# Kernel tuning notes

Measured on AMD Instinct MI355X. Metric: run time of the kernel, lower is better.

The kernel has to match this reference:

```python
import jax, jax.numpy as jnp
import numpy as np


def setup_inputs() -> dict:
    key = jax.random.key(0)
    k1, k2, k3, k4 = jax.random.split(key, 4)
    B, S, D = 32, 2048, 128
    queries = jax.random.normal(k1, (B, S, D), dtype=jnp.float32)
    keys = jax.random.normal(k2, (B, S, D), dtype=jnp.float32)
    values = jax.random.normal(k3, (B, S, D), dtype=jnp.float32)
    mask = jax.random.randint(k4, (B, 1, S), 0, 2, dtype=jnp.int32)
    return {"queries": queries, "keys": keys, "values": values, "mask": mask}


def reference(queries, keys, values, mask):
    # scores: [B, Sq, Sk]
    scores = jnp.einsum("bqd,bkd->bqk", queries, keys)
    pad = (mask == 0)  # broadcasts [B,1,Sk] over queries
    min_value = jnp.finfo(scores.dtype).min
    scores = jnp.where(pad, min_value, scores)
    attn = jax.nn.softmax(scores, axis=-1)
    attn = jnp.where(pad, jnp.array(0.0, attn.dtype), attn)
    return jnp.einsum("bqk,bkd->bqd", attn, values)
```

## Files before the change

kernel.cpp:

```cpp
#include <hip/hip_runtime.h>
#include <stdint.h>

#define Bb 32
#define Ss 2048
#define Dd 128
#define KVB 64
#define NIT (Ss / KVB)

typedef __attribute__((ext_vector_type(2))) float f32x2;
typedef __attribute__((ext_vector_type(4))) float f32x4;
typedef __attribute__((ext_vector_type(16))) float f32x16;
typedef __attribute__((ext_vector_type(8))) _Float16 f16x8;
typedef __attribute__((ext_vector_type(2))) __fp16 fp16x2;
typedef __attribute__((ext_vector_type(8))) unsigned short u16x8;
typedef __attribute__((ext_vector_type(4))) unsigned short u16x4;

union F16_8 { u16x8 u; uint32_t w[4]; f16x8 h; };
union F16_4 { u16x4 u; uint32_t w[2]; };

__device__ __forceinline__ uint32_t pk2(float a, float b) {
    union { fp16x2 h; uint32_t u; } v;
    v.h = __builtin_amdgcn_cvt_pkrtz(a, b);
    return v.u;
}

__global__ __launch_bounds__(256)
void attn_compact_idx(const int* __restrict__ M, int* __restrict__ IDXg, int* __restrict__ CNT) {
    __shared__ int scan_s[256];
    const int b = blockIdx.x, tid = threadIdx.x;
    const int* m = M + (size_t)b * Ss + tid * 8;
    int loc[8]; int csum = 0;
    {
        int4 a = *(const int4*)m;
        int4 c = *(const int4*)(m + 4);
        loc[0] = (a.x != 0); loc[1] = (a.y != 0); loc[2] = (a.z != 0); loc[3] = (a.w != 0);
        loc[4] = (c.x != 0); loc[5] = (c.y != 0); loc[6] = (c.z != 0); loc[7] = (c.w != 0);
#pragma unroll
        for (int j = 0; j < 8; ++j) csum += loc[j];
    }
    scan_s[tid] = csum;
    __syncthreads();
    for (int off = 1; off < 256; off <<= 1) {
        int v = scan_s[tid];
        int u = (tid >= off) ? scan_s[tid - off] : 0;
        __syncthreads();
        scan_s[tid] = v + u;
        __syncthreads();
    }
    int base = scan_s[tid] - csum;
    int* idx = IDXg + (size_t)b * Ss;
#pragma unroll
    for (int j = 0; j < 8; ++j)
        if (loc[j]) idx[base++] = tid * 8 + j;
    if (tid == 255) CNT[b] = scan_s[255];
}

__global__ __launch_bounds__(256)
void attn_compact_copy(const float* __restrict__ K, const float* __restrict__ V,
                       const int* __restrict__ IDXg, const int* __restrict__ CNT,
                       unsigned short* __restrict__ Kc, unsigned short* __restrict__ Vc) {
    const int b = blockIdx.x >> 5, chunk = blockIdx.x & 31;
    const int count = CNT[b];
    const int ntpad = ((count + 63) >> 6) << 6;
    const int p0 = chunk * 64;
    if (p0 >= ntpad) return;
    const int tid  = threadIdx.x;
    const int rsub = tid >> 4;
    const int colh = (tid & 15) * 8;
    const int* idx = IDXg + (size_t)b * Ss;
    const size_t gbase = (size_t)b * Ss * Dd;
#pragma unroll
    for (int pass = 0; pass < 2; ++pass) {
        const float* src = pass ? V : K;
        unsigned short* dst = pass ? Vc : Kc;
#pragma unroll
        for (int it = 0; it < 4; ++it) {
            int s = p0 + rsub + it * 16;
            if (s >= ntpad) continue;
            F16_8 t;
            if (s < count) {
                const float* sp = src + gbase + (size_t)idx[s] * Dd + colh;
                f32x4 x = *(const f32x4*)sp;
                f32x4 y = *(const f32x4*)(sp + 4);
                t.w[0] = pk2(x[0], x[1]); t.w[1] = pk2(x[2], x[3]);
                t.w[2] = pk2(y[0], y[1]); t.w[3] = pk2(y[2], y[3]);
            } else {
                t.w[0] = 0u; t.w[1] = 0u; t.w[2] = 0u; t.w[3] = 0u;
            }
            *(u16x8*)(dst + gbase + (size_t)s * Dd + colh) = t.u;
        }
    }
}

__global__ __launch_bounds__(256) __attribute__((amdgpu_waves_per_eu(2, 2)))
void attn_fwd_c(const float* __restrict__ Q,
                const unsigned short* __restrict__ Kc,
                const unsigned short* __restrict__ Vc,
                const int* __restrict__ CNT,
                float* __restrict__ O) {
    __shared__ unsigned short K_lds[KVB * 128];
    __shared__ unsigned short VT_lds[128 * 64];
    __shared__ float maskadd[KVB];

    const int tid = threadIdx.x;
    const int w   = tid >> 6;
    const int l   = tid & 63;
    const int q31 = l & 31;
    const int hi  = l >> 5;

    const int bid   = blockIdx.x;
    const int batch = (bid & 7) * 4 + (bid >> 7);
    const int qtile = (bid >> 3) & 15;

    const size_t qrow0 = (size_t)batch * Ss + qtile * 128 + w * 32;
    const size_t kvb16 = (size_t)batch * Ss * Dd;

    const int count = CNT[batch];
    const int ntile = (count + KVB - 1) >> 6;

    const int krow  = tid >> 4;
    const int kcol8 = (tid & 15) << 3;
    const int vi    = tid & 15;
    const int vk    = (tid >> 4) << 2;

    u16x8    ka[4];
    uint32_t vv[4][4];

    auto issueK = [&](int kv) {
#pragma unroll
        for (int it = 0; it < 4; ++it)
            ka[it] = *(const u16x8*)(Kc + kvb16 + (size_t)(kv + krow + it * 16) * Dd + kcol8);
    };
    auto writeK = [&](int kv) {
#pragma unroll
        for (int it = 0; it < 4; ++it) {
            int row = krow + it * 16;
            *(u16x8*)&K_lds[(row * 128 + kcol8) ^ ((row & 7) << 3)] = ka[it];
        }
        if (tid < KVB) maskadd[tid] = (kv + tid < count) ? 0.f : -1e30f;
    };
    auto issueV = [&](int kv) {
#pragma unroll
        for (int j = 0; j < 4; ++j)
#pragma unroll
            for (int ko = 0; ko < 4; ++ko)
                vv[j][ko] = *(const uint32_t*)(Vc + kvb16 + (size_t)(kv + vk + ko) * Dd + 2 * vi + 32 * j);
    };
    auto writeV = [&]() {
#pragma unroll
        for (int j = 0; j < 4; ++j)
#pragma unroll
            for (int p = 0; p < 2; ++p) {
                int row = 2 * vi + p + 32 * j;
                F16_4 t;
                if (p == 0) {
                    t.w[0] = (vv[j][0] & 0xffffu) | (vv[j][1] << 16);
                    t.w[1] = (vv[j][2] & 0xffffu) | (vv[j][3] << 16);
                } else {
                    t.w[0] = (vv[j][0] >> 16) | (vv[j][1] & 0xffff0000u);
                    t.w[1] = (vv[j][2] >> 16) | (vv[j][3] & 0xffff0000u);
                }
                *(u16x4*)&VT_lds[row * 64 + (vk ^ ((row & 7) << 3))] = t.u;
            }
    };

    F16_8 ones;
    {
        uint32_t ow = (q31 < 8) ? 0x3C003C00u : 0u;
        ones.w[0] = ow; ones.w[1] = ow; ones.w[2] = ow; ones.w[3] = ow;
    }

    const f32x16 z16 = {0,0,0,0,0,0,0,0,0,0,0,0,0,0,0,0};
    f32x16 acco[4];
#pragma unroll
    for (int dn = 0; dn < 4; ++dn) acco[dn] = z16;
    f32x16 accl = z16;
    float mrun = -1e4f;

    const float LOG2E = 1.44269504088896340736f;
    if (ntile > 0) { issueK(0); issueV(0); }
    F16_8 qf[8];
#pragma unroll
    for (int ks = 0; ks < 8; ++ks) {
        const float* s = Q + (qrow0 + q31) * Dd + ks * 16 + hi * 8;
        f32x4 a = *(const f32x4*)s;
        f32x4 b = *(const f32x4*)(s + 4);
        qf[ks].w[0] = pk2(a[0] * LOG2E, a[1] * LOG2E);
        qf[ks].w[1] = pk2(a[2] * LOG2E, a[3] * LOG2E);
        qf[ks].w[2] = pk2(b[0] * LOG2E, b[1] * LOG2E);
        qf[ks].w[3] = pk2(b[2] * LOG2E, b[3] * LOG2E);
    }
    if (ntile > 0) {
        writeK(0); writeV();
        __syncthreads();
    }

    for (int t = 0; t < ntile; ++t) {
        if (t < ntile - 1) issueK((t + 1) * KVB);

        f32x16 accs[2];
        accs[0] = z16; accs[1] = z16;
#pragma unroll
        for (int ks = 0; ks < 8; ++ks) {
#pragma unroll
            for (int n = 0; n < 2; ++n) {
                int row = n * 32 + q31;
                F16_8 kf;
                kf.u = *(const u16x8*)&K_lds[(row * 128 + ks * 16 + hi * 8) ^ ((row & 7) << 3)];
                accs[n] = __builtin_amdgcn_mfma_f32_32x32x16_f16(kf.h, qf[ks].h, accs[n], 0, 0, 0);
            }
        }

        if ((t == ntile - 1) && (count & 63)) {
#pragma unroll
            for (int n = 0; n < 2; ++n)
#pragma unroll
                for (int blk = 0; blk < 4; ++blk) {
                    f32x4 md = *(const f32x4*)&maskadd[n * 32 + blk * 8 + 4 * hi];
#pragma unroll
                    for (int r = 0; r < 4; ++r) accs[n][blk * 4 + r] += md[r];
                }
        }

        float mx[16];
#pragma unroll
        for (int i = 0; i < 16; ++i) mx[i] = fmaxf(accs[0][i], accs[1][i]);
#pragma unroll
        for (int s = 8; s >= 1; s >>= 1)
#pragma unroll
            for (int i = 0; i < s; ++i) mx[i] = fmaxf(mx[i], mx[i + s]);
        float pmax = fmaxf(mx[0], __shfl_xor(mx[0], 32));

        if (!__all(pmax - mrun <= 11.5409f)) {
            float mnew = fmaxf(mrun, pmax);
            float sc = __builtin_amdgcn_exp2f(mrun - mnew);
#pragma unroll
            for (int dn = 0; dn < 4; ++dn)
#pragma unroll
                for (int i = 0; i < 16; ++i) acco[dn][i] *= sc;
            accl[0] *= sc;
            mrun = mnew;
        }

#pragma unroll
        for (int n = 0; n < 2; ++n)
#pragma unroll
            for (int i = 0; i < 16; ++i) accs[n][i] = __builtin_amdgcn_exp2f(accs[n][i] - mrun);

        F16_8 pa[4];
#pragma unroll
        for (int ks = 0; ks < 4; ++ks) {
            int n  = ks >> 1;
            int b4 = (ks & 1) * 8;
            uint32_t x0 = pk2(accs[n][b4 + 0], accs[n][b4 + 1]);
            uint32_t x1 = pk2(accs[n][b4 + 2], accs[n][b4 + 3]);
            uint32_t y0 = pk2(accs[n][b4 + 4], accs[n][b4 + 5]);
            uint32_t y1 = pk2(accs[n][b4 + 6], accs[n][b4 + 7]);
            asm volatile("v_permlane32_swap_b32 %0, %1" : "+v"(x0), "+v"(y0));
            asm volatile("v_permlane32_swap_b32 %0, %1" : "+v"(x1), "+v"(y1));
            pa[ks].w[0] = x0; pa[ks].w[1] = x1; pa[ks].w[2] = y0; pa[ks].w[3] = y1;
        }

        __syncthreads();
        if (t < ntile - 1) { writeK((t + 1) * KVB); issueV((t + 1) * KVB); }

#pragma unroll
        for (int dn = 0; dn < 4; ++dn) {
            int row = dn * 32 + q31;
#pragma unroll
            for (int ks = 0; ks < 4; ++ks) {
                F16_8 vf;
                vf.u = *(const u16x8*)&VT_lds[row * 64 + ((ks * 16 + hi * 8) ^ ((row & 7) << 3))];
                acco[dn] = __builtin_amdgcn_mfma_f32_32x32x16_f16(vf.h, pa[ks].h, acco[dn], 0, 0, 0);
            }
        }
#pragma unroll
        for (int ks = 0; ks < 4; ++ks)
            accl = __builtin_amdgcn_mfma_f32_32x32x16_f16(ones.h, pa[ks].h, accl, 0, 0, 0);

        __syncthreads();
        if (t < ntile - 1) writeV();
    }

    float lv   = accl[0];
    float linv = lv > 0.f ? 1.0f / lv : 0.f;
    float* orow = O + (qrow0 + q31) * Dd;
#pragma unroll
    for (int dn = 0; dn < 4; ++dn)
#pragma unroll
        for (int rg = 0; rg < 4; ++rg) {
            f32x4 o;
            o[0] = acco[dn][rg * 4 + 0] * linv;
            o[1] = acco[dn][rg * 4 + 1] * linv;
            o[2] = acco[dn][rg * 4 + 2] * linv;
            o[3] = acco[dn][rg * 4 + 3] * linv;
            *(f32x4*)(orow + dn * 32 + rg * 8 + 4 * hi) = o;
        }
}

__global__ __launch_bounds__(256) __attribute__((amdgpu_waves_per_eu(2, 2)))
void attn_fwd(const float* __restrict__ Q,
              const float* __restrict__ K,
              const float* __restrict__ V,
              const int* __restrict__ M,
              float* __restrict__ O) {
    __shared__ unsigned short K_lds[KVB * 128];
    __shared__ unsigned short VT_lds[128 * 64];
    __shared__ float maskadd[KVB];

    const int tid = threadIdx.x;
    const int w   = tid >> 6;
    const int l   = tid & 63;
    const int q31 = l & 31;
    const int hi  = l >> 5;

    const int bid   = blockIdx.x;
    const int batch = (bid & 7) * 4 + (bid >> 7);
    const int qtile = (bid >> 3) & 15;

    const size_t qrow0  = (size_t)batch * Ss + qtile * 128 + w * 32;
    const size_t kvbase = (size_t)batch * Ss * Dd;
    const size_t mbase  = (size_t)batch * Ss;

    const int krow = tid >> 4;
    const int kcol = (tid & 15) << 3;
    const int vi   = tid & 15;
    const int vk   = (tid >> 4) << 2;

    f32x4 ka[4], kb[4];
    f32x2 vv[4][4];
    int mld = 0;

    auto issueK = [&](int kv) {
#pragma unroll
        for (int it = 0; it < 4; ++it) {
            const float* s = K + kvbase + (size_t)(kv + krow + it * 16) * Dd + kcol;
            ka[it] = *(const f32x4*)s;
            kb[it] = *(const f32x4*)(s + 4);
        }
        if (tid < KVB) mld = M[mbase + kv + tid];
    };
    auto writeK = [&]() {
#pragma unroll
        for (int it = 0; it < 4; ++it) {
            int row = krow + it * 16;
            F16_8 t;
            t.w[0] = pk2(ka[it][0], ka[it][1]);
            t.w[1] = pk2(ka[it][2], ka[it][3]);
            t.w[2] = pk2(kb[it][0], kb[it][1]);
            t.w[3] = pk2(kb[it][2], kb[it][3]);
            *(u16x8*)&K_lds[(row * 128 + kcol) ^ ((row & 7) << 3)] = t.u;
        }
        if (tid < KVB) maskadd[tid] = mld ? 0.f : -1e30f;
    };
    auto issueV = [&](int kv) {
#pragma unroll
        for (int j = 0; j < 4; ++j)
#pragma unroll
            for (int ko = 0; ko < 4; ++ko)
                vv[j][ko] = *(const f32x2*)(V + kvbase + (size_t)(kv + vk + ko) * Dd + 2 * vi + 32 * j);
    };
    auto writeV = [&]() {
#pragma unroll
        for (int j = 0; j < 4; ++j)
#pragma unroll
            for (int p = 0; p < 2; ++p) {
                int row = 2 * vi + p + 32 * j;
                F16_4 t;
                t.w[0] = pk2(vv[j][0][p], vv[j][1][p]);
                t.w[1] = pk2(vv[j][2][p], vv[j][3][p]);
                *(u16x4*)&VT_lds[row * 64 + (vk ^ ((row & 7) << 3))] = t.u;
            }
    };

    F16_8 ones;
    {
        uint32_t ow = (q31 < 8) ? 0x3C003C00u : 0u;
        ones.w[0] = ow; ones.w[1] = ow; ones.w[2] = ow; ones.w[3] = ow;
    }

    const f32x16 z16 = {0,0,0,0,0,0,0,0,0,0,0,0,0,0,0,0};
    f32x16 acco[4];
#pragma unroll
    for (int dn = 0; dn < 4; ++dn) acco[dn] = z16;
    f32x16 accl = z16;
    float mrun = -1e4f;

    const float LOG2E = 1.44269504088896340736f;
    issueK(0); issueV(0);
    F16_8 qf[8];
#pragma unroll
    for (int ks = 0; ks < 8; ++ks) {
        const float* s = Q + (qrow0 + q31) * Dd + ks * 16 + hi * 8;
        f32x4 a = *(const f32x4*)s;
        f32x4 b = *(const f32x4*)(s + 4);
        qf[ks].w[0] = pk2(a[0] * LOG2E, a[1] * LOG2E);
        qf[ks].w[1] = pk2(a[2] * LOG2E, a[3] * LOG2E);
        qf[ks].w[2] = pk2(b[0] * LOG2E, b[1] * LOG2E);
        qf[ks].w[3] = pk2(b[2] * LOG2E, b[3] * LOG2E);
    }
    writeK(); writeV();
    __syncthreads();

    for (int t = 0; t < NIT; ++t) {
        if (t < NIT - 1) issueK((t + 1) * KVB);

        f32x16 accs[2];
        accs[0] = z16; accs[1] = z16;
#pragma unroll
        for (int ks = 0; ks < 8; ++ks) {
#pragma unroll
            for (int n = 0; n < 2; ++n) {
                int row = n * 32 + q31;
                F16_8 kf;
                kf.u = *(const u16x8*)&K_lds[(row * 128 + ks * 16 + hi * 8) ^ ((row & 7) << 3)];
                accs[n] = __builtin_amdgcn_mfma_f32_32x32x16_f16(kf.h, qf[ks].h, accs[n], 0, 0, 0);
            }
        }

#pragma unroll
        for (int n = 0; n < 2; ++n)
#pragma unroll
            for (int blk = 0; blk < 4; ++blk) {
                f32x4 md = *(const f32x4*)&maskadd[n * 32 + blk * 8 + 4 * hi];
#pragma unroll
                for (int r = 0; r < 4; ++r) accs[n][blk * 4 + r] += md[r];
            }

        float mx[16];
#pragma unroll
        for (int i = 0; i < 16; ++i) mx[i] = fmaxf(accs[0][i], accs[1][i]);
#pragma unroll
        for (int s = 8; s >= 1; s >>= 1)
#pragma unroll
            for (int i = 0; i < s; ++i) mx[i] = fmaxf(mx[i], mx[i + s]);
        float pmax = fmaxf(mx[0], __shfl_xor(mx[0], 32));

        if (!__all(pmax - mrun <= 11.5409f)) {
            float mnew = fmaxf(mrun, pmax);
            float sc = __builtin_amdgcn_exp2f(mrun - mnew);
#pragma unroll
            for (int dn = 0; dn < 4; ++dn)
#pragma unroll
                for (int i = 0; i < 16; ++i) acco[dn][i] *= sc;
            accl[0] *= sc;
            mrun = mnew;
        }

#pragma unroll
        for (int n = 0; n < 2; ++n)
#pragma unroll
            for (int i = 0; i < 16; ++i) accs[n][i] = __builtin_amdgcn_exp2f(accs[n][i] - mrun);

        F16_8 pa[4];
#pragma unroll
        for (int ks = 0; ks < 4; ++ks) {
            int n  = ks >> 1;
            int b4 = (ks & 1) * 8;
            uint32_t x0 = pk2(accs[n][b4 + 0], accs[n][b4 + 1]);
            uint32_t x1 = pk2(accs[n][b4 + 2], accs[n][b4 + 3]);
            uint32_t y0 = pk2(accs[n][b4 + 4], accs[n][b4 + 5]);
            uint32_t y1 = pk2(accs[n][b4 + 6], accs[n][b4 + 7]);
            asm volatile("v_permlane32_swap_b32 %0, %1" : "+v"(x0), "+v"(y0));
            asm volatile("v_permlane32_swap_b32 %0, %1" : "+v"(x1), "+v"(y1));
            pa[ks].w[0] = x0; pa[ks].w[1] = x1; pa[ks].w[2] = y0; pa[ks].w[3] = y1;
        }

        __syncthreads();
        if (t < NIT - 1) { writeK(); issueV((t + 1) * KVB); }

#pragma unroll
        for (int dn = 0; dn < 4; ++dn) {
            int row = dn * 32 + q31;
#pragma unroll
            for (int ks = 0; ks < 4; ++ks) {
                F16_8 vf;
                vf.u = *(const u16x8*)&VT_lds[row * 64 + ((ks * 16 + hi * 8) ^ ((row & 7) << 3))];
                acco[dn] = __builtin_amdgcn_mfma_f32_32x32x16_f16(vf.h, pa[ks].h, acco[dn], 0, 0, 0);
            }
        }
#pragma unroll
        for (int ks = 0; ks < 4; ++ks)
            accl = __builtin_amdgcn_mfma_f32_32x32x16_f16(ones.h, pa[ks].h, accl, 0, 0, 0);

        __syncthreads();
        if (t < NIT - 1) writeV();
    }

    float lv   = accl[0];
    float linv = lv > 0.f ? 1.0f / lv : 0.f;
    float* orow = O + (qrow0 + q31) * Dd;
#pragma unroll
    for (int dn = 0; dn < 4; ++dn)
#pragma unroll
        for (int rg = 0; rg < 4; ++rg) {
            f32x4 o;
            o[0] = acco[dn][rg * 4 + 0] * linv;
            o[1] = acco[dn][rg * 4 + 1] * linv;
            o[2] = acco[dn][rg * 4 + 2] * linv;
            o[3] = acco[dn][rg * 4 + 3] * linv;
            *(f32x4*)(orow + dn * 32 + rg * 8 + 4 * hi) = o;
        }
}

extern "C" void kernel_launch(void* const* d_in, const int* in_sizes, int n_in,
                              void* d_out, int out_size, void* d_ws, size_t ws_size,
                              hipStream_t stream) {
    const float* Q = (const float*)d_in[0];
    const float* K = (const float*)d_in[1];
    const float* V = (const float*)d_in[2];
    const int*   M = (const int*)d_in[3];
    float* O = (float*)d_out;

    const size_t nKV   = (size_t)Bb * Ss * Dd;
    const size_t need  = nKV * 2 * 2 + (size_t)Bb * Ss * 4 + Bb * 4;

    if (d_ws != nullptr && ws_size >= need) {
        unsigned short* Kc   = (unsigned short*)d_ws;
        unsigned short* Vc   = Kc + nKV;
        int*            IDXg = (int*)(Vc + nKV);
        int*            CNT  = IDXg + (size_t)Bb * Ss;
        attn_compact_idx<<<dim3(Bb), dim3(256), 0, stream>>>(M, IDXg, CNT);
        attn_compact_copy<<<dim3(Bb * 32), dim3(256), 0, stream>>>(K, V, IDXg, CNT, Kc, Vc);
        attn_fwd_c<<<dim3(Bb * (Ss / 128)), dim3(256), 0, stream>>>(Q, Kc, Vc, CNT, O);
    } else {
        attn_fwd<<<dim3(Bb * (Ss / 128)), dim3(256), 0, stream>>>(Q, K, V, M, O);
    }
}
```

Before: 75.75 us.

## Fuse K/V gather and fp16 conversion into attention kernel, drop compact copy

Removes the separate kernel that gathered unmasked K/V rows into compacted fp16 buffers. The attention kernel now loads a per-batch index list (stored as uint16) into LDS and gathers fp32 K/V rows directly, converting them to fp16 when writing to LDS. This saves one launch and the write-then-read round trip of the compacted K/V. In exchange, K/V are re-read in fp32 by each of the 16 query tiles, doubling per-load bytes, and the gathers are indirect. It also adds 4KB of LDS per block.

```diff
diff --git a/kernel.cpp b/kernel.cpp
--- a/kernel.cpp
+++ b/kernel.cpp
@@ -25,7 +25,8 @@
 }
 
 __global__ __launch_bounds__(256)
-void attn_compact_idx(const int* __restrict__ M, int* __restrict__ IDXg, int* __restrict__ CNT) {
+void attn_compact_idx(const int* __restrict__ M, unsigned short* __restrict__ IDXg,
+                      int* __restrict__ CNT) {
     __shared__ int scan_s[256];
     const int b = blockIdx.x, tid = threadIdx.x;
     const int* m = M + (size_t)b * Ss + tid * 8;
@@ -47,60 +48,27 @@
         scan_s[tid] = v + u;
         __syncthreads();
     }
+    const int count = scan_s[255];
     int base = scan_s[tid] - csum;
-    int* idx = IDXg + (size_t)b * Ss;
+    unsigned short* idx = IDXg + (size_t)b * Ss;
 #pragma unroll
     for (int j = 0; j < 8; ++j)
-        if (loc[j]) idx[base++] = tid * 8 + j;
-    if (tid == 255) CNT[b] = scan_s[255];
+        if (loc[j]) idx[base++] = (unsigned short)(tid * 8 + j);
+    for (int p = count + tid; p < Ss; p += 256) idx[p] = 0;
+    if (tid == 0) CNT[b] = count;
 }
 
-__global__ __launch_bounds__(256)
-void attn_compact_copy(const float* __restrict__ K, const float* __restrict__ V,
-                       const int* __restrict__ IDXg, const int* __restrict__ CNT,
-                       unsigned short* __restrict__ Kc, unsigned short* __restrict__ Vc) {
-    const int b = blockIdx.x >> 5, chunk = blockIdx.x & 31;
-    const int count = CNT[b];
-    const int ntpad = ((count + 63) >> 6) << 6;
-    const int p0 = chunk * 64;
-    if (p0 >= ntpad) return;
-    const int tid  = threadIdx.x;
-    const int rsub = tid >> 4;
-    const int colh = (tid & 15) * 8;
-    const int* idx = IDXg + (size_t)b * Ss;
-    const size_t gbase = (size_t)b * Ss * Dd;
-#pragma unroll
-    for (int pass = 0; pass < 2; ++pass) {
-        const float* src = pass ? V : K;
-        unsigned short* dst = pass ? Vc : Kc;
-#pragma unroll
-        for (int it = 0; it < 4; ++it) {
-            int s = p0 + rsub + it * 16;
-            if (s >= ntpad) continue;
-            F16_8 t;
-            if (s < count) {
-                const float* sp = src + gbase + (size_t)idx[s] * Dd + colh;
-                f32x4 x = *(const f32x4*)sp;
-                f32x4 y = *(const f32x4*)(sp + 4);
-                t.w[0] = pk2(x[0], x[1]); t.w[1] = pk2(x[2], x[3]);
-                t.w[2] = pk2(y[0], y[1]); t.w[3] = pk2(y[2], y[3]);
-            } else {
-                t.w[0] = 0u; t.w[1] = 0u; t.w[2] = 0u; t.w[3] = 0u;
-            }
-            *(u16x8*)(dst + gbase + (size_t)s * Dd + colh) = t.u;
-        }
-    }
-}
-
 __global__ __launch_bounds__(256) __attribute__((amdgpu_waves_per_eu(2, 2)))
-void attn_fwd_c(const float* __restrict__ Q,
-                const unsigned short* __restrict__ Kc,
-                const unsigned short* __restrict__ Vc,
+void attn_fwd_g(const float* __restrict__ Q,
+                const float* __restrict__ K,
+                const float* __restrict__ V,
+                const unsigned short* __restrict__ IDXg,
                 const int* __restrict__ CNT,
                 float* __restrict__ O) {
     __shared__ unsigned short K_lds[KVB * 128];
     __shared__ unsigned short VT_lds[128 * 64];
     __shared__ float maskadd[KVB];
+    __shared__ unsigned short IDX_lds[Ss];
 
     const int tid = threadIdx.x;
     const int w   = tid >> 6;
@@ -112,39 +80,54 @@
     const int batch = (bid & 7) * 4 + (bid >> 7);
     const int qtile = (bid >> 3) & 15;
 
-    const size_t qrow0 = (size_t)batch * Ss + qtile * 128 + w * 32;
-    const size_t kvb16 = (size_t)batch * Ss * Dd;
+    const size_t qrow0  = (size_t)batch * Ss + qtile * 128 + w * 32;
+    const size_t kvbase = (size_t)batch * Ss * Dd;
 
     const int count = CNT[batch];
     const int ntile = (count + KVB - 1) >> 6;
 
-    const int krow  = tid >> 4;
-    const int kcol8 = (tid & 15) << 3;
-    const int vi    = tid & 15;
-    const int vk    = (tid >> 4) << 2;
-
-    u16x8    ka[4];
-    uint32_t vv[4][4];
+    *(u16x8*)&IDX_lds[tid * 8] = *(const u16x8*)(IDXg + (size_t)batch * Ss + tid * 8);
+    __syncthreads();
+
+    const int krow = tid >> 4;
+    const int kcol = (tid & 15) << 3;
+    const int vi   = tid & 15;
+    const int vk   = (tid >> 4) << 2;
+
+    f32x4 ka[4], kb[4];
+    f32x2 vv[4][4];
 
     auto issueK = [&](int kv) {
 #pragma unroll
-        for (int it = 0; it < 4; ++it)
-            ka[it] = *(const u16x8*)(Kc + kvb16 + (size_t)(kv + krow + it * 16) * Dd + kcol8);
+        for (int it = 0; it < 4; ++it) {
+            const int r = IDX_lds[kv + krow + it * 16];
+            const float* s = K + kvbase + (size_t)r * Dd + kcol;
+            ka[it] = *(const f32x4*)s;
+            kb[it] = *(const f32x4*)(s + 4);
+        }
     };
     auto writeK = [&](int kv) {
 #pragma unroll
         for (int it = 0; it < 4; ++it) {
             int row = krow + it * 16;
-            *(u16x8*)&K_lds[(row * 128 + kcol8) ^ ((row & 7) << 3)] = ka[it];
+            F16_8 t;
+            t.w[0] = pk2(ka[it][0], ka[it][1]);
+            t.w[1] = pk2(ka[it][2], ka[it][3]);
+            t.w[2] = pk2(kb[it][0], kb[it][1]);
+            t.w[3] = pk2(kb[it][2], kb[it][3]);
+            *(u16x8*)&K_lds[(row * 128 + kcol) ^ ((row & 7) << 3)] = t.u;
         }
         if (tid < KVB) maskadd[tid] = (kv + tid < count) ? 0.f : -1e30f;
     };
     auto issueV = [&](int kv) {
+        int rr[4];
+#pragma unroll
+        for (int ko = 0; ko < 4; ++ko) rr[ko] = IDX_lds[kv + vk + ko];
 #pragma unroll
         for (int j = 0; j < 4; ++j)
 #pragma unroll
             for (int ko = 0; ko < 4; ++ko)
-                vv[j][ko] = *(const uint32_t*)(Vc + kvb16 + (size_t)(kv + vk + ko) * Dd + 2 * vi + 32 * j);
+                vv[j][ko] = *(const f32x2*)(V + kvbase + (size_t)rr[ko] * Dd + 2 * vi + 32 * j);
     };
     auto writeV = [&]() {
 #pragma unroll
@@ -153,13 +136,8 @@
             for (int p = 0; p < 2; ++p) {
                 int row = 2 * vi + p + 32 * j;
                 F16_4 t;
-                if (p == 0) {
-                    t.w[0] = (vv[j][0] & 0xffffu) | (vv[j][1] << 16);
-                    t.w[1] = (vv[j][2] & 0xffffu) | (vv[j][3] << 16);
-                } else {
-                    t.w[0] = (vv[j][0] >> 16) | (vv[j][1] & 0xffff0000u);
-                    t.w[1] = (vv[j][2] >> 16) | (vv[j][3] & 0xffff0000u);
-                }
+                t.w[0] = pk2(vv[j][0][p], vv[j][1][p]);
+                t.w[1] = pk2(vv[j][2][p], vv[j][3][p]);
                 *(u16x4*)&VT_lds[row * 64 + (vk ^ ((row & 7) << 3))] = t.u;
             }
     };
@@ -512,17 +490,13 @@
     const int*   M = (const int*)d_in[3];
     float* O = (float*)d_out;
 
-    const size_t nKV   = (size_t)Bb * Ss * Dd;
-    const size_t need  = nKV * 2 * 2 + (size_t)Bb * Ss * 4 + Bb * 4;
+    const size_t need = (size_t)Bb * Ss * 2 + (size_t)Bb * 4;
 
     if (d_ws != nullptr && ws_size >= need) {
-        unsigned short* Kc   = (unsigned short*)d_ws;
-        unsigned short* Vc   = Kc + nKV;
-        int*            IDXg = (int*)(Vc + nKV);
-        int*            CNT  = IDXg + (size_t)Bb * Ss;
+        unsigned short* IDXg = (unsigned short*)d_ws;
+        int*            CNT  = (int*)(IDXg + (size_t)Bb * Ss);
         attn_compact_idx<<<dim3(Bb), dim3(256), 0, stream>>>(M, IDXg, CNT);
-        attn_compact_copy<<<dim3(Bb * 32), dim3(256), 0, stream>>>(K, V, IDXg, CNT, Kc, Vc);
-        attn_fwd_c<<<dim3(Bb * (Ss / 128)), dim3(256), 0, stream>>>(Q, Kc, Vc, CNT, O);
+        attn_fwd_g<<<dim3(Bb * (Ss / 128)), dim3(256), 0, stream>>>(Q, K, V, IDXg, CNT, O);
     } else {
         attn_fwd<<<dim3(Bb * (Ss / 128)), dim3(256), 0, stream>>>(Q, K, V, M, O);
     }
```

New measurement: 130.8 us. 1.73x slower.

## Fuse mask compaction into gather kernel and double-buffer K/V via direct LDS loads

Applied to the files above, without the earlier changes.

Merges the index-compaction and K/V gather kernels into one kernel where each block recomputes the mask prefix scan and keeps indices in shared memory, removing a launch and the global index buffer. The attention kernel now double-buffers K and V tiles in LDS, loading K with global_load_lds directly into a swizzled layout and dropping one barrier per iteration. The mask-add is computed once for the last tile instead of per tile. The cost is redundant scans across the 32 blocks per batch and doubled LDS usage, which may affect occupancy.

```diff
diff --git a/kernel.cpp b/kernel.cpp
--- a/kernel.cpp
+++ b/kernel.cpp
@@ -25,9 +25,15 @@
 }
 
 __global__ __launch_bounds__(256)
-void attn_compact_idx(const int* __restrict__ M, int* __restrict__ IDXg, int* __restrict__ CNT) {
+void attn_prep(const float* __restrict__ K, const float* __restrict__ V,
+               const int* __restrict__ M,
+               unsigned short* __restrict__ Kc, unsigned short* __restrict__ Vc,
+               int* __restrict__ CNT) {
     __shared__ int scan_s[256];
-    const int b = blockIdx.x, tid = threadIdx.x;
+    __shared__ unsigned short idx_l[Ss];
+    const int b = blockIdx.x >> 5, chunk = blockIdx.x & 31;
+    const int tid = threadIdx.x;
+
     const int* m = M + (size_t)b * Ss + tid * 8;
     int loc[8]; int csum = 0;
     {
@@ -47,27 +53,22 @@
         scan_s[tid] = v + u;
         __syncthreads();
     }
-    int base = scan_s[tid] - csum;
-    int* idx = IDXg + (size_t)b * Ss;
-#pragma unroll
-    for (int j = 0; j < 8; ++j)
-        if (loc[j]) idx[base++] = tid * 8 + j;
-    if (tid == 255) CNT[b] = scan_s[255];
-}
-
-__global__ __launch_bounds__(256)
-void attn_compact_copy(const float* __restrict__ K, const float* __restrict__ V,
-                       const int* __restrict__ IDXg, const int* __restrict__ CNT,
-                       unsigned short* __restrict__ Kc, unsigned short* __restrict__ Vc) {
-    const int b = blockIdx.x >> 5, chunk = blockIdx.x & 31;
-    const int count = CNT[b];
+    const int count = scan_s[255];
+    {
+        int base = scan_s[tid] - csum;
+#pragma unroll
+        for (int j = 0; j < 8; ++j)
+            if (loc[j]) idx_l[base++] = (unsigned short)(tid * 8 + j);
+    }
+    __syncthreads();
+    if (chunk == 0 && tid == 0) CNT[b] = count;
+
     const int ntpad = ((count + 63) >> 6) << 6;
     const int p0 = chunk * 64;
     if (p0 >= ntpad) return;
-    const int tid  = threadIdx.x;
+
     const int rsub = tid >> 4;
     const int colh = (tid & 15) * 8;
-    const int* idx = IDXg + (size_t)b * Ss;
     const size_t gbase = (size_t)b * Ss * Dd;
 #pragma unroll
     for (int pass = 0; pass < 2; ++pass) {
@@ -79,7 +80,7 @@
             if (s >= ntpad) continue;
             F16_8 t;
             if (s < count) {
-                const float* sp = src + gbase + (size_t)idx[s] * Dd + colh;
+                const float* sp = src + gbase + (size_t)idx_l[s] * Dd + colh;
                 f32x4 x = *(const f32x4*)sp;
                 f32x4 y = *(const f32x4*)(sp + 4);
                 t.w[0] = pk2(x[0], x[1]); t.w[1] = pk2(x[2], x[3]);
@@ -93,13 +94,13 @@
 }
 
 __global__ __launch_bounds__(256) __attribute__((amdgpu_waves_per_eu(2, 2)))
-void attn_fwd_c(const float* __restrict__ Q,
+void attn_fwd_d(const float* __restrict__ Q,
                 const unsigned short* __restrict__ Kc,
                 const unsigned short* __restrict__ Vc,
                 const int* __restrict__ CNT,
                 float* __restrict__ O) {
-    __shared__ unsigned short K_lds[KVB * 128];
-    __shared__ unsigned short VT_lds[128 * 64];
+    __shared__ unsigned short K_lds[2][KVB * 128];
+    __shared__ unsigned short VT_lds[2][128 * 64];
     __shared__ float maskadd[KVB];
 
     const int tid = threadIdx.x;
@@ -118,27 +119,24 @@
     const int count = CNT[batch];
     const int ntile = (count + KVB - 1) >> 6;
 
-    const int krow  = tid >> 4;
-    const int kcol8 = (tid & 15) << 3;
-    const int vi    = tid & 15;
-    const int vk    = (tid >> 4) << 2;
-
-    u16x8    ka[4];
+    const int grow = tid >> 4;
+    const int gs   = tid & 15;
+    auto gloadK = [&](int bf, int kv) {
+#pragma unroll
+        for (int it = 0; it < 4; ++it) {
+            const int r = it * 16 + grow;
+            const unsigned short* src = Kc + kvb16 + (size_t)(kv + r) * Dd + ((gs ^ (r & 7)) << 3);
+            void* dst = (char*)(&K_lds[bf][0]) + it * 4096 + w * 1024;
+            __builtin_amdgcn_global_load_lds(
+                (const __attribute__((address_space(1))) uint32_t*)src,
+                (__attribute__((address_space(3))) uint32_t*)dst, 16, 0, 0);
+        }
+    };
+
+    const int vi = tid & 15;
+    const int vk = (tid >> 4) << 2;
     uint32_t vv[4][4];
 
-    auto issueK = [&](int kv) {
-#pragma unroll
-        for (int it = 0; it < 4; ++it)
-            ka[it] = *(const u16x8*)(Kc + kvb16 + (size_t)(kv + krow + it * 16) * Dd + kcol8);
-    };
-    auto writeK = [&](int kv) {
-#pragma unroll
-        for (int it = 0; it < 4; ++it) {
-            int row = krow + it * 16;
-            *(u16x8*)&K_lds[(row * 128 + kcol8) ^ ((row & 7) << 3)] = ka[it];
-        }
-        if (tid < KVB) maskadd[tid] = (kv + tid < count) ? 0.f : -1e30f;
-    };
     auto issueV = [&](int kv) {
 #pragma unroll
         for (int j = 0; j < 4; ++j)
@@ -146,7 +144,7 @@
             for (int ko = 0; ko < 4; ++ko)
                 vv[j][ko] = *(const uint32_t*)(Vc + kvb16 + (size_t)(kv + vk + ko) * Dd + 2 * vi + 32 * j);
     };
-    auto writeV = [&]() {
+    auto writeV = [&](int bf) {
 #pragma unroll
         for (int j = 0; j < 4; ++j)
 #pragma unroll
@@ -160,7 +158,7 @@
                     t.w[0] = (vv[j][0] >> 16) | (vv[j][1] & 0xffff0000u);
                     t.w[1] = (vv[j][2] >> 16) | (vv[j][3] & 0xffff0000u);
                 }
-                *(u16x4*)&VT_lds[row * 64 + (vk ^ ((row & 7) << 3))] = t.u;
+                *(u16x4*)&VT_lds[bf][row * 64 + (vk ^ ((row & 7) << 3))] = t.u;
             }
     };
 
@@ -178,7 +176,8 @@
     float mrun = -1e4f;
 
     const float LOG2E = 1.44269504088896340736f;
-    if (ntile > 0) { issueK(0); issueV(0); }
+    if (ntile > 0) { gloadK(0, 0); issueV(0); }
+    if (tid < KVB) maskadd[tid] = ((ntile - 1) * KVB + tid < count) ? 0.f : -1e30f;
     F16_8 qf[8];
 #pragma unroll
     for (int ks = 0; ks < 8; ++ks) {
@@ -191,12 +190,14 @@
         qf[ks].w[3] = pk2(b[2] * LOG2E, b[3] * LOG2E);
     }
     if (ntile > 0) {
-        writeK(0); writeV();
+        writeV(0);
         __syncthreads();
     }
 
     for (int t = 0; t < ntile; ++t) {
-        if (t < ntile - 1) issueK((t + 1) * KVB);
+        const int bf = t & 1;
+        const bool pf = (t + 1 < ntile);
+        if (pf) { gloadK(bf ^ 1, (t + 1) * KVB); issueV((t + 1) * KVB); }
 
         f32x16 accs[2];
         accs[0] = z16; accs[1] = z16;
@@ -206,7 +207,7 @@
             for (int n = 0; n < 2; ++n) {
                 int row = n * 32 + q31;
                 F16_8 kf;
-                kf.u = *(const u16x8*)&K_lds[(row * 128 + ks * 16 + hi * 8) ^ ((row & 7) << 3)];
+                kf.u = *(const u16x8*)&K_lds[bf][(row * 128 + ks * 16 + hi * 8) ^ ((row & 7) << 3)];
                 accs[n] = __builtin_amdgcn_mfma_f32_32x32x16_f16(kf.h, qf[ks].h, accs[n], 0, 0, 0);
             }
         }
@@ -261,8 +262,7 @@
             pa[ks].w[0] = x0; pa[ks].w[1] = x1; pa[ks].w[2] = y0; pa[ks].w[3] = y1;
         }
 
-        __syncthreads();
-        if (t < ntile - 1) { writeK((t + 1) * KVB); issueV((t + 1) * KVB); }
+        if (pf) writeV(bf ^ 1);
 
 #pragma unroll
         for (int dn = 0; dn < 4; ++dn) {
@@ -270,7 +270,7 @@
 #pragma unroll
             for (int ks = 0; ks < 4; ++ks) {
                 F16_8 vf;
-                vf.u = *(const u16x8*)&VT_lds[row * 64 + ((ks * 16 + hi * 8) ^ ((row & 7) << 3))];
+                vf.u = *(const u16x8*)&VT_lds[bf][row * 64 + ((ks * 16 + hi * 8) ^ ((row & 7) << 3))];
                 acco[dn] = __builtin_amdgcn_mfma_f32_32x32x16_f16(vf.h, pa[ks].h, acco[dn], 0, 0, 0);
             }
         }
@@ -278,8 +278,7 @@
         for (int ks = 0; ks < 4; ++ks)
             accl = __builtin_amdgcn_mfma_f32_32x32x16_f16(ones.h, pa[ks].h, accl, 0, 0, 0);
 
-        __syncthreads();
-        if (t < ntile - 1) writeV();
+        if (pf) __syncthreads();
     }
 
     float lv   = accl[0];
@@ -512,17 +511,15 @@
     const int*   M = (const int*)d_in[3];
     float* O = (float*)d_out;
 
-    const size_t nKV   = (size_t)Bb * Ss * Dd;
-    const size_t need  = nKV * 2 * 2 + (size_t)Bb * Ss * 4 + Bb * 4;
+    const size_t nKV  = (size_t)Bb * Ss * Dd;
+    const size_t need = nKV * 2 * 2 + (size_t)Bb * 4;
 
     if (d_ws != nullptr && ws_size >= need) {
-        unsigned short* Kc   = (unsigned short*)d_ws;
-        unsigned short* Vc   = Kc + nKV;
-        int*            IDXg = (int*)(Vc + nKV);
-        int*            CNT  = IDXg + (size_t)Bb * Ss;
-        attn_compact_idx<<<dim3(Bb), dim3(256), 0, stream>>>(M, IDXg, CNT);
-        attn_compact_copy<<<dim3(Bb * 32), dim3(256), 0, stream>>>(K, V, IDXg, CNT, Kc, Vc);
-        attn_fwd_c<<<dim3(Bb * (Ss / 128)), dim3(256), 0, stream>>>(Q, Kc, Vc, CNT, O);
+        unsigned short* Kc  = (unsigned short*)d_ws;
+        unsigned short* Vc  = Kc + nKV;
+        int*            CNT = (int*)(Vc + nKV);
+        attn_prep<<<dim3(Bb * 32), dim3(256), 0, stream>>>(K, V, M, Kc, Vc, CNT);
+        attn_fwd_d<<<dim3(Bb * (Ss / 128)), dim3(256), 0, stream>>>(Q, Kc, Vc, CNT, O);
     } else {
         attn_fwd<<<dim3(Bb * (Ss / 128)), dim3(256), 0, stream>>>(Q, K, V, M, O);
     }
```

Result: faster. 69.61 us (-8.1%).
